# Kernel optimization log

Hardware: AMD Instinct MI355X
Metric: run time of the kernel (lower is better)

## Reference

```python
import jax, jax.numpy as jnp
import numpy as np

CUTOFF = 6.0
NWAVE = 12
NTYPE = 2
DIMS = [36, 256, 128, 64, 32, 1]  # norbit -> hidden -> output


def setup_inputs() -> dict:
    key = jax.random.key(0)
    N, K = 8192, 48
    M = N * K
    ks = jax.random.split(key, 16)
    cart = jax.random.uniform(ks[0], (N, 3), jnp.float32, 0.0, 40.0)
    species = jax.random.randint(ks[1], (N,), 0, NTYPE).astype(jnp.int32)
    center = jnp.repeat(jnp.arange(N, dtype=jnp.int32), K)          # row 0: center atom i
    off = jax.random.randint(ks[2], (M,), 1, N).astype(jnp.int32)
    neigh = jnp.mod(center + off, N)                                 # row 1: neighbor j != i
    neigh_list = jnp.stack([center, neigh], axis=0)
    shifts = jax.random.normal(ks[3], (M, 3), jnp.float32)           # PBC shift vectors
    rs = jnp.tile(jnp.linspace(0.0, CUTOFF, NWAVE, dtype=jnp.float32), (NTYPE, 1))
    inta = -0.5 * jnp.ones((NTYPE, NWAVE), jnp.float32)              # gaussian exponents (negative)
    cparams = jnp.ones((NTYPE, NWAVE), jnp.float32)                  # embedded-atom coefficients
    params = {}
    kidx = 4
    for i in range(4):  # 4 hidden layers, stacked over [3 nets, ntype]
        fi, fo = DIMS[i], DIMS[i + 1]
        params[f'w{i+1}'] = jax.random.normal(ks[kidx], (3, NTYPE, fi, fo), jnp.float32) / np.sqrt(fi)
        params[f'b{i+1}'] = jnp.zeros((3, NTYPE, fo), jnp.float32)
        params[f'a{i+1}'] = jnp.ones((3, NTYPE, fo), jnp.float32)    # Relu_like alpha
        params[f'g{i+1}'] = jnp.ones((3, NTYPE, fo), jnp.float32)    # Relu_like beta
        kidx += 1
    params['wout'] = jax.random.normal(ks[kidx], (3, NTYPE, DIMS[4], 1), jnp.float32) / np.sqrt(DIMS[4])
    params['bout'] = jnp.zeros((3, NTYPE, 1), jnp.float32)
    return dict(cart=cart, shifts=shifts, rs=rs, inta=inta, cparams=cparams,
                **params, species=species, neigh_list=neigh_list)


def density_fn(cart, shifts, rs, inta, cparams, species, neigh_list):
    # EANN GetDensity: radial gaussians * cosine cutoff * angular monomials, scattered to centers.
    N = cart.shape[0]
    i, j = neigh_list[0], neigh_list[1]
    dvec = cart[i] - cart[j] + shifts                                 # [M,3]
    dist = jnp.linalg.norm(dvec, axis=-1)                             # [M]
    fc = jnp.square(0.5 * jnp.cos(dist * (jnp.pi / CUTOFF)) + 0.5)    # cutoff_cosine
    # angular basis: L=0 (1), L=1 (3), L=2 (9) -> 13 components, each premultiplied by fc
    ang = jnp.concatenate([
        fc[:, None],
        fc[:, None] * dvec,
        fc[:, None] * (dvec[:, :, None] * dvec[:, None, :]).reshape(-1, 9),
    ], axis=1)                                                        # [M,13]
    sj = species[j]
    gauss = jnp.exp(inta[sj] * jnp.square(dist[:, None] - rs[sj])) * cparams[sj]  # [M,NWAVE]
    worb = ang[:, :, None] * gauss[:, None, :]                        # [M,13,NWAVE]
    B = jax.ops.segment_sum(worb, i, num_segments=N)                  # [N,13,NWAVE]
    d0 = jnp.square(B[:, 0])                                          # L=0
    d1 = jnp.sum(jnp.square(B[:, 1:4]), axis=1)                       # L=1
    d2 = jnp.sum(jnp.square(B[:, 4:13]), axis=1)                      # L=2
    return jnp.concatenate([d0, d1, d2], axis=1)                      # [N,36]


def net_energy(density, species, layers, wout, bout):
    # per-atom-type MLP with Relu_like activation a*silu(g*x); run all types, select by species
    T = wout.shape[0]
    h = jnp.broadcast_to(density, (T,) + density.shape)               # [T,N,36]
    for (w, b, a, g) in layers:
        h = jnp.einsum('tnf,tfo->tno', h, w) + b[:, None, :]
        h = a[:, None, :] * jax.nn.silu(g[:, None, :] * h)
    out = jnp.einsum('tnf,tfo->tno', h, wout) + bout[:, None, :]      # [T,N,1]
    per_atom = jnp.take_along_axis(out[..., 0].T, species[:, None].astype(jnp.int32), axis=1)[:, 0]
    return jnp.sum(per_atom)


def reference(cart, shifts, rs, inta, cparams,
              w1, b1, a1, g1, w2, b2, a2, g2, w3, b3, a3, g3, w4, b4, a4, g4,
              wout, bout, species, neigh_list):
    def energy(c, n):
        d = density_fn(c, shifts, rs, inta, cparams, species, neigh_list)
        layers = [(w1[n], b1[n], a1[n], g1[n]), (w2[n], b2[n], a2[n], g2[n]),
                  (w3[n], b3[n], a3[n], g3[n]), (w4[n], b4[n], a4[n], g4[n])]
        return net_energy(d, species, layers, wout[n], bout[n])

    jab1 = jax.grad(lambda c: energy(c, 0))(cart)                     # dE0/dcart (create_graph analogue)
    jab2 = jax.grad(lambda c: energy(c, 1))(cart)                     # dE1/dcart
    e2 = energy(cart, 2)
    polar = jnp.einsum('ij,ik->jk', cart, jab1)
    polar = polar + polar.T + jnp.einsum('ij,ik->jk', jab2, jab2)
    polar = polar + e2 * jnp.eye(3, dtype=polar.dtype)
    return polar
```

## Files before the change

### kernel.cpp

```cpp
#include <hip/hip_runtime.h>

#define NWAVE 12
#define NL 13
#define NBW (NL*NWAVE)
#define D0 36
#define D1 256
#define D2 128
#define D3 64
#define D4 32
#define AT 16
#define NMAX 8192
#define NBSC 128
#define PI6 0.52359877559829887307f

#define F4(p) (*(const float4*)(p))
#define F2(p) (*(const float2*)(p))

__device__ __forceinline__ float wave_reduce(float v){
  #pragma unroll
  for(int o=32;o>0;o>>=1) v += __shfl_down(v,o);
  return v;
}

__global__ void perm_kernel(const int* __restrict__ species, int* __restrict__ perm,
                            int* __restrict__ counts, int N){
  __shared__ int sc[256];
  int t = threadIdx.x;
  int per = N/256;
  int c0 = 0;
  for(int k=0;k<per;k++) c0 += (species[t*per+k]==0) ? 1 : 0;
  sc[t]=c0; __syncthreads();
  for(int off=1; off<256; off<<=1){
    int add = (t>=off)? sc[t-off] : 0;
    __syncthreads();
    sc[t] += add;
    __syncthreads();
  }
  int incl = sc[t];
  int excl = incl - c0;
  int total0 = sc[255];
  if(t==0){ counts[0]=total0; counts[1]=N-total0; }
  int base0 = excl;
  int base1 = N + (t*per - excl);
  for(int k=0;k<per;k++){
    int a = t*per+k;
    if(species[a]==0) perm[base0++]=a; else perm[base1++]=a;
  }
}

__global__ void transpose_kernel(const float* __restrict__ src, float* __restrict__ dst,
                                 int fi, int fo, int cpb){
  int slab = blockIdx.x / cpb;
  int chunk = blockIdx.x % cpb;
  int idx = chunk*256 + threadIdx.x;
  int E = fi*fo;
  if(idx < E){
    int f = idx / fo, o = idx % fo;
    dst[slab*E + o*fi + f] = src[slab*E + idx];
  }
}

__global__ void pairs_kernel(const float* __restrict__ cart, const float* __restrict__ shifts,
                             const int* __restrict__ species, const int* __restrict__ neighJ,
                             float4* __restrict__ pairbuf, int M, int N, int K){
  extern __shared__ float4 ca[];
  int t = threadIdx.x;
  for(int a=t; a<N; a+=blockDim.x)
    ca[a] = make_float4(cart[a*3+0], cart[a*3+1], cart[a*3+2], (float)species[a]);
  __syncthreads();
  int stride = gridDim.x*blockDim.x;
  for(int m = blockIdx.x*blockDim.x + t; m < M; m += stride){
    int i = m / K;
    int j = neighJ[m];
    float4 cj = ca[j];
    float4 ci = ca[i];
    float dx = ci.x - cj.x + shifts[m*3+0];
    float dy = ci.y - cj.y + shifts[m*3+1];
    float dz = ci.z - cj.z + shifts[m*3+2];
    float dist = sqrtf(dx*dx+dy*dy+dz*dz);
    float enc = (cj.w != 0.f) ? -dist : dist;
    pairbuf[m] = make_float4(dx, dy, dz, enc);
  }
}

__launch_bounds__(64)
__global__ void density_kernel(const float4* __restrict__ pairbuf,
                               const float* __restrict__ rs, const float* __restrict__ inta,
                               const float* __restrict__ cparams,
                               float* __restrict__ B, int K){
  int i = blockIdx.x;
  int t = threadIdx.x;
  __shared__ float sang[64][NL];
  __shared__ float sg[64][NWAVE];
  if(t < K){
    float4 pb = pairbuf[(size_t)i*K + t];
    float dx = pb.x, dy = pb.y, dz = pb.z;
    int sj = (pb.w < 0.f) ? 1 : 0;
    float dist = fabsf(pb.w);
    float base = 0.5f*cosf(dist*PI6)+0.5f;
    float fc = base*base;
    #pragma unroll
    for(int w=0;w<NWAVE;w++){
      float d = dist - rs[sj*NWAVE+w];
      sg[t][w] = __expf(inta[sj*NWAVE+w]*d*d)*cparams[sj*NWAVE+w];
    }
    sang[t][0]=fc;
    sang[t][1]=fc*dx;  sang[t][2]=fc*dy;  sang[t][3]=fc*dz;
    sang[t][4]=fc*dx*dx; sang[t][5]=fc*dx*dy; sang[t][6]=fc*dx*dz;
    sang[t][7]=fc*dy*dx; sang[t][8]=fc*dy*dy; sang[t][9]=fc*dy*dz;
    sang[t][10]=fc*dz*dx; sang[t][11]=fc*dz*dy; sang[t][12]=fc*dz*dz;
  }
  __syncthreads();
  for(int idx=t; idx<NBW; idx+=64){
    int l = idx/NWAVE, w = idx%NWAVE;
    float s = 0.f;
    for(int k=0;k<K;k++) s += sang[k][l]*sg[k][w];
    B[i*NBW+idx] = s;
  }
}

__launch_bounds__(256, 1)
__global__ void mlp_kernel(const float* __restrict__ B,
    const int* __restrict__ perm, const int* __restrict__ counts,
    const float* __restrict__ w1,const float* __restrict__ b1,const float* __restrict__ a1,const float* __restrict__ g1,
    const float* __restrict__ w2,const float* __restrict__ b2,const float* __restrict__ a2,const float* __restrict__ g2,
    const float* __restrict__ w3,const float* __restrict__ b3,const float* __restrict__ a3,const float* __restrict__ g3,
    const float* __restrict__ w4,const float* __restrict__ b4,const float* __restrict__ a4,const float* __restrict__ g4,
    const float* __restrict__ wout,const float* __restrict__ bout,
    const float* __restrict__ wt1,const float* __restrict__ wt2,const float* __restrict__ wt3,const float* __restrict__ wt4,
    float* __restrict__ G1, float* __restrict__ G2, float* __restrict__ e2acc, int N)
{
  const int bpt = N/AT;
  const int net = blockIdx.x / (2*bpt);
  const int rem = blockIdx.x % (2*bpt);
  const int typ = rem / bpt;
  const int sbase = (rem % bpt)*AT;
  const int cnt = counts[typ];
  if(sbase >= cnt) return;
  const int tid = threadIdx.x;
  const int slab = net*2 + typ;

  __shared__ __align__(16) float X[AT][D0];
  __shared__ __align__(16) float H1s[AT*D1];
  __shared__ __align__(16) float H2s[AT*D2];
  __shared__ __align__(16) float H3s[AT*D3];
  __shared__ __align__(16) float H4s[AT*D4];
  __shared__ int atomsS[AT];

  if(tid < AT){
    int slot = sbase + tid;
    atomsS[tid] = (slot < cnt) ? perm[typ*N + slot] : -1;
  }
  __syncthreads();

  for(int idx=tid; idx<AT*D0; idx+=256){
    int r = idx/D0, f = idx%D0;
    int a = atomsS[r];
    float v = 0.f;
    if(a >= 0){
      int w = f%NWAVE, grp = f/NWAVE;
      const float* Br = B + a*NBW;
      if(grp==0){ float b0=Br[w]; v=b0*b0; }
      else if(grp==1){
        #pragma unroll
        for(int l=1;l<4;l++){ float b0=Br[l*NWAVE+w]; v += b0*b0; }
      } else {
        #pragma unroll
        for(int l=4;l<13;l++){ float b0=Br[l*NWAVE+w]; v += b0*b0; }
      }
    }
    X[r][f] = v;
  }
  __syncthreads();

  const int l1c = (tid & 63)*4,  l1r = (tid >> 6)*4;
  const int l2c = (tid & 63)*2,  l2r = (tid >> 6)*4;
  const int l3c = (tid & 31)*2,  l3r = (tid >> 5)*2;
  const int l4c = (tid & 31),    l4r = (tid >> 5)*2;

  float A1r[4][4], A2r[4][2], A3r[2][2], A4r[2];

  {
    const float* W = w1 + slab*D0*D1;
    float acc[4][4];
    {
      float4 bv = F4(&b1[slab*D1+l1c]);
      #pragma unroll
      for(int rr=0;rr<4;rr++){ acc[rr][0]=bv.x; acc[rr][1]=bv.y; acc[rr][2]=bv.z; acc[rr][3]=bv.w; }
    }
    #pragma unroll
    for(int kk=0; kk<D0/4; kk++){
      float4 wa = F4(&W[(kk*4+0)*D1+l1c]);
      float4 wb = F4(&W[(kk*4+1)*D1+l1c]);
      float4 wc = F4(&W[(kk*4+2)*D1+l1c]);
      float4 wd = F4(&W[(kk*4+3)*D1+l1c]);
      #pragma unroll
      for(int rr=0;rr<4;rr++){
        float4 xv = F4(&X[l1r+rr][kk*4]);
        acc[rr][0] += xv.x*wa.x + xv.y*wb.x + xv.z*wc.x + xv.w*wd.x;
        acc[rr][1] += xv.x*wa.y + xv.y*wb.y + xv.z*wc.y + xv.w*wd.y;
        acc[rr][2] += xv.x*wa.z + xv.y*wb.z + xv.z*wc.z + xv.w*wd.z;
        acc[rr][3] += xv.x*wa.w + xv.y*wb.w + xv.z*wc.w + xv.w*wd.w;
      }
    }
    float4 av4 = F4(&a1[slab*D1+l1c]);
    float4 gv4 = F4(&g1[slab*D1+l1c]);
    float avv[4] = {av4.x, av4.y, av4.z, av4.w};
    float gvv[4] = {gv4.x, gv4.y, gv4.z, gv4.w};
    #pragma unroll
    for(int rr=0;rr<4;rr++){
      float4 h;
      float hp[4];
      #pragma unroll
      for(int cc=0;cc<4;cc++){
        float u = gvv[cc]*acc[rr][cc];
        float s = 1.f/(1.f+__expf(-u));
        hp[cc] = avv[cc]*u*s;
        A1r[rr][cc] = avv[cc]*gvv[cc]*s*(1.f + u*(1.f-s));
      }
      h.x=hp[0]; h.y=hp[1]; h.z=hp[2]; h.w=hp[3];
      *(float4*)&H1s[(l1r+rr)*D1 + l1c] = h;
    }
  }
  __syncthreads();
  {
    const float* W = w2 + slab*D1*D2;
    float acc[4][2];
    {
      float2 bv = F2(&b2[slab*D2+l2c]);
      #pragma unroll
      for(int rr=0;rr<4;rr++){ acc[rr][0]=bv.x; acc[rr][1]=bv.y; }
    }
    for(int kk=0; kk<D1/4; kk++){
      float2 wa = F2(&W[(kk*4+0)*D2+l2c]);
      float2 wb = F2(&W[(kk*4+1)*D2+l2c]);
      float2 wc = F2(&W[(kk*4+2)*D2+l2c]);
      float2 wd = F2(&W[(kk*4+3)*D2+l2c]);
      #pragma unroll
      for(int rr=0;rr<4;rr++){
        float4 hv = F4(&H1s[(l2r+rr)*D1 + kk*4]);
        acc[rr][0] += hv.x*wa.x + hv.y*wb.x + hv.z*wc.x + hv.w*wd.x;
        acc[rr][1] += hv.x*wa.y + hv.y*wb.y + hv.z*wc.y + hv.w*wd.y;
      }
    }
    float2 av2 = F2(&a2[slab*D2+l2c]);
    float2 gv2 = F2(&g2[slab*D2+l2c]);
    float avv[2] = {av2.x, av2.y};
    float gvv[2] = {gv2.x, gv2.y};
    #pragma unroll
    for(int rr=0;rr<4;rr++){
      float hp[2];
      #pragma unroll
      for(int cc=0;cc<2;cc++){
        float u = gvv[cc]*acc[rr][cc];
        float s = 1.f/(1.f+__expf(-u));
        hp[cc] = avv[cc]*u*s;
        A2r[rr][cc] = avv[cc]*gvv[cc]*s*(1.f + u*(1.f-s));
      }
      float2 h; h.x=hp[0]; h.y=hp[1];
      *(float2*)&H2s[(l2r+rr)*D2 + l2c] = h;
    }
  }
  __syncthreads();
  {
    const float* W = w3 + slab*D2*D3;
    float acc[2][2];
    {
      float2 bv = F2(&b3[slab*D3+l3c]);
      #pragma unroll
      for(int rr=0;rr<2;rr++){ acc[rr][0]=bv.x; acc[rr][1]=bv.y; }
    }
    for(int kk=0; kk<D2/4; kk++){
      float2 wa = F2(&W[(kk*4+0)*D3+l3c]);
      float2 wb = F2(&W[(kk*4+1)*D3+l3c]);
      float2 wc = F2(&W[(kk*4+2)*D3+l3c]);
      float2 wd = F2(&W[(kk*4+3)*D3+l3c]);
      #pragma unroll
      for(int rr=0;rr<2;rr++){
        float4 hv = F4(&H2s[(l3r+rr)*D2 + kk*4]);
        acc[rr][0] += hv.x*wa.x + hv.y*wb.x + hv.z*wc.x + hv.w*wd.x;
        acc[rr][1] += hv.x*wa.y + hv.y*wb.y + hv.z*wc.y + hv.w*wd.y;
      }
    }
    float2 av2 = F2(&a3[slab*D3+l3c]);
    float2 gv2 = F2(&g3[slab*D3+l3c]);
    float avv[2] = {av2.x, av2.y};
    float gvv[2] = {gv2.x, gv2.y};
    #pragma unroll
    for(int rr=0;rr<2;rr++){
      float hp[2];
      #pragma unroll
      for(int cc=0;cc<2;cc++){
        float u = gvv[cc]*acc[rr][cc];
        float s = 1.f/(1.f+__expf(-u));
        hp[cc] = avv[cc]*u*s;
        A3r[rr][cc] = avv[cc]*gvv[cc]*s*(1.f + u*(1.f-s));
      }
      float2 h; h.x=hp[0]; h.y=hp[1];
      *(float2*)&H3s[(l3r+rr)*D3 + l3c] = h;
    }
  }
  __syncthreads();
  {
    const float* W = w4 + slab*D3*D4;
    float bias = b4[slab*D4+l4c];
    float acc[2] = {bias, bias};
    for(int kk=0; kk<D3/4; kk++){
      float wa = W[(kk*4+0)*D4+l4c];
      float wb = W[(kk*4+1)*D4+l4c];
      float wc = W[(kk*4+2)*D4+l4c];
      float wd = W[(kk*4+3)*D4+l4c];
      #pragma unroll
      for(int rr=0;rr<2;rr++){
        float4 hv = F4(&H3s[(l4r+rr)*D3 + kk*4]);
        acc[rr] += hv.x*wa + hv.y*wb + hv.z*wc + hv.w*wd;
      }
    }
    float av = a4[slab*D4+l4c], gv = g4[slab*D4+l4c];
    #pragma unroll
    for(int rr=0;rr<2;rr++){
      float u = gv*acc[rr];
      float s = 1.f/(1.f+__expf(-u));
      H4s[(l4r+rr)*D4+l4c] = av*u*s;
      A4r[rr] = av*gv*s*(1.f + u*(1.f-s));
    }
  }
  __syncthreads();
  {
    const float* wo = wout + slab*D4;
    float val = 0.f;
    if(tid < AT){
      float s = bout[slab];
      const float* hr = &H4s[tid*D4];
      #pragma unroll
      for(int f=0;f<D4;f++) s += hr[f]*wo[f];
      if(net==2 && atomsS[tid]>=0) val = s;
    }
    if(net==2 && tid < 64){
      float v = wave_reduce(val);
      if(tid==0) atomicAdd(e2acc, v);
    }
  }
  if(net < 2){
    float* __restrict__ Gout = (net==0)? G1 : G2;
    const float* wo = wout + slab*D4;
    __syncthreads();
    {
      float wv = wo[l4c];
      H3s[(l4r+0)*D4+l4c] = wv * A4r[0];
      H3s[(l4r+1)*D4+l4c] = wv * A4r[1];
    }
    __syncthreads();
    {
      const float* WT = wt4 + slab*D4*D3;
      float acc[2][2] = {{0.f,0.f},{0.f,0.f}};
      #pragma unroll
      for(int kk=0; kk<D4/4; kk++){
        float2 wa = F2(&WT[(kk*4+0)*D3+l3c]);
        float2 wb = F2(&WT[(kk*4+1)*D3+l3c]);
        float2 wc = F2(&WT[(kk*4+2)*D3+l3c]);
        float2 wd = F2(&WT[(kk*4+3)*D3+l3c]);
        #pragma unroll
        for(int rr=0;rr<2;rr++){
          float4 dv = F4(&H3s[(l3r+rr)*D4 + kk*4]);
          acc[rr][0] += dv.x*wa.x + dv.y*wb.x + dv.z*wc.x + dv.w*wd.x;
          acc[rr][1] += dv.x*wa.y + dv.y*wb.y + dv.z*wc.y + dv.w*wd.y;
        }
      }
      #pragma unroll
      for(int rr=0;rr<2;rr++){
        float2 h;
        h.x = acc[rr][0]*A3r[rr][0];
        h.y = acc[rr][1]*A3r[rr][1];
        *(float2*)&H1s[(l3r+rr)*D3 + l3c] = h;
      }
    }
    __syncthreads();
    {
      const float* WT = wt3 + slab*D3*D2;
      float acc[4][2] = {{0.f,0.f},{0.f,0.f},{0.f,0.f},{0.f,0.f}};
      for(int kk=0; kk<D3/4; kk++){
        float2 wa = F2(&WT[(kk*4+0)*D2+l2c]);
        float2 wb = F2(&WT[(kk*4+1)*D2+l2c]);
        float2 wc = F2(&WT[(kk*4+2)*D2+l2c]);
        float2 wd = F2(&WT[(kk*4+3)*D2+l2c]);
        #pragma unroll
        for(int rr=0;rr<4;rr++){
          float4 dv = F4(&H1s[(l2r+rr)*D3 + kk*4]);
          acc[rr][0] += dv.x*wa.x + dv.y*wb.x + dv.z*wc.x + dv.w*wd.x;
          acc[rr][1] += dv.x*wa.y + dv.y*wb.y + dv.z*wc.y + dv.w*wd.y;
        }
      }
      #pragma unroll
      for(int rr=0;rr<4;rr++){
        float2 h;
        h.x = acc[rr][0]*A2r[rr][0];
        h.y = acc[rr][1]*A2r[rr][1];
        *(float2*)&H2s[(l2r+rr)*D2 + l2c] = h;
      }
    }
    __syncthreads();
    {
      const float* WT = wt2 + slab*D2*D1;
      float acc[4][4];
      #pragma unroll
      for(int rr=0;rr<4;rr++){ acc[rr][0]=0.f; acc[rr][1]=0.f; acc[rr][2]=0.f; acc[rr][3]=0.f; }
      for(int kk=0; kk<D2/4; kk++){
        float4 wa = F4(&WT[(kk*4+0)*D1+l1c]);
        float4 wb = F4(&WT[(kk*4+1)*D1+l1c]);
        float4 wc = F4(&WT[(kk*4+2)*D1+l1c]);
        float4 wd = F4(&WT[(kk*4+3)*D1+l1c]);
        #pragma unroll
        for(int rr=0;rr<4;rr++){
          float4 dv = F4(&H2s[(l1r+rr)*D2 + kk*4]);
          acc[rr][0] += dv.x*wa.x + dv.y*wb.x + dv.z*wc.x + dv.w*wd.x;
          acc[rr][1] += dv.x*wa.y + dv.y*wb.y + dv.z*wc.y + dv.w*wd.y;
          acc[rr][2] += dv.x*wa.z + dv.y*wb.z + dv.z*wc.z + dv.w*wd.z;
          acc[rr][3] += dv.x*wa.w + dv.y*wb.w + dv.z*wc.w + dv.w*wd.w;
        }
      }
      #pragma unroll
      for(int rr=0;rr<4;rr++){
        float4 h;
        h.x = acc[rr][0]*A1r[rr][0];
        h.y = acc[rr][1]*A1r[rr][1];
        h.z = acc[rr][2]*A1r[rr][2];
        h.w = acc[rr][3]*A1r[rr][3];
        *(float4*)&H1s[(l1r+rr)*D1 + l1c] = h;
      }
    }
    __syncthreads();
    {
      const float* WT = wt1 + slab*D1*D0;
      for(int idx=tid; idx<AT*D0; idx+=256){
        int r = idx/D0, f = idx%D0;
        const float* dr = &H1s[r*D1];
        float acc = 0.f;
        for(int oo=0; oo<D1; oo+=4){
          const float4 dv = F4(&dr[oo]);
          acc += dv.x*WT[(oo+0)*D0+f] + dv.y*WT[(oo+1)*D0+f]
               + dv.z*WT[(oo+2)*D0+f] + dv.w*WT[(oo+3)*D0+f];
        }
        int a = atomsS[r];
        if(a >= 0) Gout[a*D0+f] = acc;
      }
    }
  }
}

__launch_bounds__(64)
__global__ void pair_back_kernel(const float4* __restrict__ pairbuf,
                                 const float* __restrict__ shifts,
                                 const float* __restrict__ rs, const float* __restrict__ inta,
                                 const float* __restrict__ cparams,
                                 const float* __restrict__ B,
                                 const float* __restrict__ G1, const float* __restrict__ G2,
                                 float* __restrict__ Ppart, float* __restrict__ jab2c,
                                 float* __restrict__ f2buf, int K){
  int i = blockIdx.x;
  int t = threadIdx.x;
  __shared__ float E1[NBW], E2[NBW];
  for(int idx=t; idx<NBW; idx+=64){
    int l = idx/NWAVE, w = idx%NWAVE;
    int grp = (l==0) ? 0 : ((l<4) ? 1 : 2);
    float b = B[i*NBW+idx];
    E1[idx] = 2.f*b*G1[i*D0 + grp*NWAVE + w];
    E2[idx] = 2.f*b*G2[i*D0 + grp*NWAVE + w];
  }
  __syncthreads();
  float p[9] = {0.f,0.f,0.f,0.f,0.f,0.f,0.f,0.f,0.f};
  float fi2[3] = {0.f,0.f,0.f};
  if(t < K){
    int m = i*K + t;
    float4 pb = pairbuf[(size_t)m];
    float dx = pb.x, dy = pb.y, dz = pb.z;
    int sj = (pb.w < 0.f) ? 1 : 0;
    float dist = fabsf(pb.w);
    float shx = shifts[m*3+0], shy = shifts[m*3+1], shz = shifts[m*3+2];
    float invd = 1.f/dist;
    float u = dist*PI6;
    float base = 0.5f*cosf(u)+0.5f;
    float fc = base*base;
    float fcp = -PI6*sinf(u)*base;
    float gs[NWAVE], tw[NWAVE];
    #pragma unroll
    for(int w=0;w<NWAVE;w++){
      float d = dist - rs[sj*NWAVE+w];
      float ia = inta[sj*NWAVE+w];
      float g = __expf(ia*d*d)*cparams[sj*NWAVE+w];
      gs[w] = g;
      tw[w] = fcp*g + fc*(2.f*ia*d*g);
    }
    float mono[NL] = {1.f, dx,dy,dz, dx*dx,dx*dy,dx*dz, dy*dx,dy*dy,dy*dz, dz*dx,dz*dy,dz*dz};
    float f1[3], f2[3];
    for(int net=0; net<2; net++){
      const float* E = net ? E2 : E1;
      float sl[NL];
      float radial = 0.f;
      #pragma unroll
      for(int l=0;l<NL;l++){
        float s = 0.f, q = 0.f;
        #pragma unroll
        for(int w=0;w<NWAVE;w++){
          float e = E[l*NWAVE+w];
          s += e*gs[w];
          q += e*tw[w];
        }
        sl[l] = s;
        radial += mono[l]*q;
      }
      float Ax = sl[1] + 2.f*sl[4]*dx + (sl[5]+sl[7])*dy + (sl[6]+sl[10])*dz;
      float Ay = sl[2] + (sl[5]+sl[7])*dx + 2.f*sl[8]*dy + (sl[9]+sl[11])*dz;
      float Az = sl[3] + (sl[6]+sl[10])*dx + (sl[9]+sl[11])*dy + 2.f*sl[12]*dz;
      float rr = radial*invd;
      float fx = dx*rr + fc*Ax;
      float fy = dy*rr + fc*Ay;
      float fz = dz*rr + fc*Az;
      if(net==0){ f1[0]=fx; f1[1]=fy; f1[2]=fz; }
      else      { f2[0]=fx; f2[1]=fy; f2[2]=fz; }
    }
    float cx = dx-shx, cy = dy-shy, cz = dz-shz;
    p[0]=cx*f1[0]; p[1]=cx*f1[1]; p[2]=cx*f1[2];
    p[3]=cy*f1[0]; p[4]=cy*f1[1]; p[5]=cy*f1[2];
    p[6]=cz*f1[0]; p[7]=cz*f1[1]; p[8]=cz*f1[2];
    float* fb = f2buf + (size_t)m*3;
    fb[0]=f2[0]; fb[1]=f2[1]; fb[2]=f2[2];
    fi2[0]=f2[0]; fi2[1]=f2[1]; fi2[2]=f2[2];
  }
  #pragma unroll
  for(int k=0;k<9;k++){
    float v = wave_reduce(p[k]);
    if(t==0) Ppart[(size_t)i*9+k] = v;
  }
  #pragma unroll
  for(int c=0;c<3;c++){
    float v = wave_reduce(fi2[c]);
    if(t==0) jab2c[(size_t)i*3+c] = v;
  }
}

__global__ void scatter_kernel(const int* __restrict__ neighJ, const float* __restrict__ f2buf,
                               float* __restrict__ jpart, int M, int N){
  __shared__ float lds[NMAX];
  int b = blockIdx.x, t = threadIdx.x;
  int chunk = (M + gridDim.x - 1) / gridDim.x;
  int m0 = b*chunk;
  int m1 = m0 + chunk; if(m1 > M) m1 = M;
  for(int c=0;c<3;c++){
    for(int n=t; n<N; n+=256) lds[n] = 0.f;
    __syncthreads();
    for(int m=m0+t; m<m1; m+=256)
      atomicAdd(&lds[neighJ[m]], -f2buf[(size_t)m*3+c]);
    __syncthreads();
    float* dst = jpart + ((size_t)b*3 + c)*N;
    for(int n=t; n<N; n+=256) dst[n] = lds[n];
    __syncthreads();
  }
}

__global__ void reduce_kernel(const float* __restrict__ Ppart, const float* __restrict__ jab2c,
                              const float* __restrict__ jpart,
                              float* __restrict__ Pacc, float* __restrict__ S2, int N){
  __shared__ float red[256];
  int tid = threadIdx.x;
  float s2[9] = {0.f,0.f,0.f,0.f,0.f,0.f,0.f,0.f,0.f};
  float pp[9] = {0.f,0.f,0.f,0.f,0.f,0.f,0.f,0.f,0.f};
  for(int n = blockIdx.x*256 + tid; n < N; n += gridDim.x*256){
    float x = jab2c[n*3+0], y = jab2c[n*3+1], z = jab2c[n*3+2];
    for(int b=0;b<NBSC;b++){
      const float* jp = jpart + (size_t)b*3*N;
      x += jp[0*(size_t)N + n];
      y += jp[1*(size_t)N + n];
      z += jp[2*(size_t)N + n];
    }
    s2[0]+=x*x; s2[1]+=x*y; s2[2]+=x*z;
    s2[3]+=y*x; s2[4]+=y*y; s2[5]+=y*z;
    s2[6]+=z*x; s2[7]+=z*y; s2[8]+=z*z;
    const float* pr = Ppart + (size_t)n*9;
    #pragma unroll
    for(int k=0;k<9;k++) pp[k] += pr[k];
  }
  #pragma unroll
  for(int k=0;k<9;k++){
    red[tid]=s2[k]; __syncthreads();
    for(int off=128; off>0; off>>=1){
      if(tid<off) red[tid]+=red[tid+off];
      __syncthreads();
    }
    if(tid==0) atomicAdd(&S2[k], red[0]);
    __syncthreads();
    red[tid]=pp[k]; __syncthreads();
    for(int off=128; off>0; off>>=1){
      if(tid<off) red[tid]+=red[tid+off];
      __syncthreads();
    }
    if(tid==0) atomicAdd(&Pacc[k], red[0]);
    __syncthreads();
  }
}

__global__ void final_kernel(const float* __restrict__ Pacc, const float* __restrict__ S2,
                             const float* __restrict__ e2acc, float* __restrict__ out){
  int tid = threadIdx.x;
  if(tid < 9){
    int a = tid/3, b = tid%3;
    float v = Pacc[a*3+b] + Pacc[b*3+a] + S2[tid];
    if(a==b) v += e2acc[0];
    out[tid] = v;
  }
}

extern "C" void kernel_launch(void* const* d_in, const int* in_sizes, int n_in,
                              void* d_out, int out_size, void* d_ws, size_t ws_size,
                              hipStream_t stream){
  const float* cart    = (const float*)d_in[0];
  const float* shifts  = (const float*)d_in[1];
  const float* rs      = (const float*)d_in[2];
  const float* inta    = (const float*)d_in[3];
  const float* cparams = (const float*)d_in[4];
  const float* w1 = (const float*)d_in[5];
  const float* b1 = (const float*)d_in[6];
  const float* a1 = (const float*)d_in[7];
  const float* g1 = (const float*)d_in[8];
  const float* w2 = (const float*)d_in[9];
  const float* b2 = (const float*)d_in[10];
  const float* a2 = (const float*)d_in[11];
  const float* g2 = (const float*)d_in[12];
  const float* w3 = (const float*)d_in[13];
  const float* b3 = (const float*)d_in[14];
  const float* a3 = (const float*)d_in[15];
  const float* g3 = (const float*)d_in[16];
  const float* w4 = (const float*)d_in[17];
  const float* b4 = (const float*)d_in[18];
  const float* a4 = (const float*)d_in[19];
  const float* g4 = (const float*)d_in[20];
  const float* wout = (const float*)d_in[21];
  const float* bout = (const float*)d_in[22];
  const int* species = (const int*)d_in[23];
  const int* neigh   = (const int*)d_in[24];
  float* out = (float*)d_out;

  const int N = in_sizes[0]/3;
  const int M = in_sizes[24]/2;
  const int K = M/N;
  const int* neighJ = neigh + M;

  char* base = (char*)d_ws;
  size_t off = 0;
  auto alloc = [&](size_t bytes)->void*{
    void* p = base + off;
    off = (off + bytes + 255) & ~(size_t)255;
    return p;
  };
  float*  Bws    = (float*)alloc((size_t)N*NBW*4);
  float*  G1ws   = (float*)alloc((size_t)N*D0*4);
  float*  G2ws   = (float*)alloc((size_t)N*D0*4);
  float*  Ppart  = (float*)alloc((size_t)N*9*4);
  float*  jab2c  = (float*)alloc((size_t)N*3*4);
  float*  f2buf  = (float*)alloc((size_t)M*3*4);
  float4* pairbuf= (float4*)alloc((size_t)M*16);
  float*  jpart  = (float*)alloc((size_t)NBSC*3*N*4);
  float*  acc    = (float*)alloc(32*4);
  int*    counts = (int*)alloc(2*4);
  int*    perm   = (int*)alloc((size_t)2*N*4);
  float*  WT1    = (float*)alloc((size_t)6*D0*D1*4);
  float*  WT2    = (float*)alloc((size_t)6*D1*D2*4);
  float*  WT3    = (float*)alloc((size_t)6*D2*D3*4);
  float*  WT4    = (float*)alloc((size_t)6*D3*D4*4);

  hipMemsetAsync(acc, 0, 32*4, stream);

  size_t ldsBytes = (size_t)N*16;
  hipFuncSetAttribute((const void*)pairs_kernel,
                      hipFuncAttributeMaxDynamicSharedMemorySize, (int)ldsBytes);

  perm_kernel<<<1,256,0,stream>>>(species, perm, counts, N);
  transpose_kernel<<<6*((D0*D1+255)/256),256,0,stream>>>(w1, WT1, D0, D1, (D0*D1+255)/256);
  transpose_kernel<<<6*((D1*D2+255)/256),256,0,stream>>>(w2, WT2, D1, D2, (D1*D2+255)/256);
  transpose_kernel<<<6*((D2*D3+255)/256),256,0,stream>>>(w3, WT3, D2, D3, (D2*D3+255)/256);
  transpose_kernel<<<6*((D3*D4+255)/256),256,0,stream>>>(w4, WT4, D3, D4, (D3*D4+255)/256);
  pairs_kernel<<<256,1024,ldsBytes,stream>>>(cart, shifts, species, neighJ, pairbuf, M, N, K);
  density_kernel<<<N,64,0,stream>>>(pairbuf, rs, inta, cparams, Bws, K);
  mlp_kernel<<<3*2*(N/AT),256,0,stream>>>(Bws, perm, counts,
      w1,b1,a1,g1, w2,b2,a2,g2, w3,b3,a3,g3, w4,b4,a4,g4, wout,bout,
      WT1,WT2,WT3,WT4, G1ws,G2ws, acc+18, N);
  pair_back_kernel<<<N,64,0,stream>>>(pairbuf, shifts, rs, inta, cparams,
                                      Bws, G1ws, G2ws, Ppart, jab2c, f2buf, K);
  scatter_kernel<<<NBSC,256,0,stream>>>(neighJ, f2buf, jpart, M, N);
  reduce_kernel<<<64,256,0,stream>>>(Ppart, jab2c, jpart, acc, acc+9, N);
  final_kernel<<<1,64,0,stream>>>(acc, acc+9, acc+18, out);
}
```

Measured before the change: 324.2 us.

## Double MLP block threads to 512 and merge weight transposes into one launch

The MLP kernel now runs 512 threads per block instead of 256. Each thread handles half as many atom rows in every forward and backward layer, which raises parallelism and cuts per-thread register use; the launch bounds change to (512,4) so more blocks can share a compute unit. The four weight-transpose launches are merged into one kernel that picks its layer by global index, removing three launch overheads. The cost is less register-level reuse of each weight load across rows, so more weight traffic goes to global memory or cache.

```diff
diff --git a/kernel.cpp b/kernel.cpp
--- a/kernel.cpp
+++ b/kernel.cpp
@@ -48,15 +48,28 @@
   }
 }
 
-__global__ void transpose_kernel(const float* __restrict__ src, float* __restrict__ dst,
-                                 int fi, int fo, int cpb){
-  int slab = blockIdx.x / cpb;
-  int chunk = blockIdx.x % cpb;
-  int idx = chunk*256 + threadIdx.x;
-  int E = fi*fo;
-  if(idx < E){
-    int f = idx / fo, o = idx % fo;
-    dst[slab*E + o*fi + f] = src[slab*E + idx];
+__global__ void transpose_all_kernel(const float* __restrict__ w1, const float* __restrict__ w2,
+                                     const float* __restrict__ w3, const float* __restrict__ w4,
+                                     float* __restrict__ t1, float* __restrict__ t2,
+                                     float* __restrict__ t3, float* __restrict__ t4){
+  const int E1 = 6*D0*D1, E2 = 6*D1*D2, E3 = 6*D2*D3, E4 = 6*D3*D4;
+  int idx = blockIdx.x*256 + threadIdx.x;
+  if(idx < E1){
+    int slab = idx/(D0*D1), r = idx%(D0*D1);
+    int f = r/D1, o = r%D1;
+    t1[slab*D0*D1 + o*D0 + f] = w1[idx];
+  } else if(idx < E1+E2){
+    int k = idx-E1; int slab = k/(D1*D2), r = k%(D1*D2);
+    int f = r/D2, o = r%D2;
+    t2[slab*D1*D2 + o*D1 + f] = w2[k];
+  } else if(idx < E1+E2+E3){
+    int k = idx-E1-E2; int slab = k/(D2*D3), r = k%(D2*D3);
+    int f = r/D3, o = r%D3;
+    t3[slab*D2*D3 + o*D2 + f] = w3[k];
+  } else if(idx < E1+E2+E3+E4){
+    int k = idx-E1-E2-E3; int slab = k/(D3*D4), r = k%(D3*D4);
+    int f = r/D4, o = r%D4;
+    t4[slab*D3*D4 + o*D3 + f] = w4[k];
   }
 }
 
@@ -119,7 +132,7 @@
   }
 }
 
-__launch_bounds__(256, 1)
+__launch_bounds__(512, 4)
 __global__ void mlp_kernel(const float* __restrict__ B,
     const int* __restrict__ perm, const int* __restrict__ counts,
     const float* __restrict__ w1,const float* __restrict__ b1,const float* __restrict__ a1,const float* __restrict__ g1,
@@ -153,7 +166,7 @@
   }
   __syncthreads();
 
-  for(int idx=tid; idx<AT*D0; idx+=256){
+  for(int idx=tid; idx<AT*D0; idx+=512){
     int r = idx/D0, f = idx%D0;
     int a = atomsS[r];
     float v = 0.f;
@@ -173,20 +186,20 @@
   }
   __syncthreads();
 
-  const int l1c = (tid & 63)*4,  l1r = (tid >> 6)*4;
-  const int l2c = (tid & 63)*2,  l2r = (tid >> 6)*4;
-  const int l3c = (tid & 31)*2,  l3r = (tid >> 5)*2;
-  const int l4c = (tid & 31),    l4r = (tid >> 5)*2;
-
-  float A1r[4][4], A2r[4][2], A3r[2][2], A4r[2];
+  const int l1c = (tid & 63)*4,  l1r = (tid >> 6)*2;
+  const int l2c = (tid & 63)*2,  l2r = (tid >> 6)*2;
+  const int l3c = (tid & 31)*2,  l3r = (tid >> 5);
+  const int l4c = (tid & 31),    l4r = (tid >> 5);
+
+  float A1r[2][4], A2r[2][2], A3r[2], A4r;
 
   {
     const float* W = w1 + slab*D0*D1;
-    float acc[4][4];
+    float acc[2][4];
     {
       float4 bv = F4(&b1[slab*D1+l1c]);
       #pragma unroll
-      for(int rr=0;rr<4;rr++){ acc[rr][0]=bv.x; acc[rr][1]=bv.y; acc[rr][2]=bv.z; acc[rr][3]=bv.w; }
+      for(int rr=0;rr<2;rr++){ acc[rr][0]=bv.x; acc[rr][1]=bv.y; acc[rr][2]=bv.z; acc[rr][3]=bv.w; }
     }
     #pragma unroll
     for(int kk=0; kk<D0/4; kk++){
@@ -195,7 +208,7 @@
       float4 wc = F4(&W[(kk*4+2)*D1+l1c]);
       float4 wd = F4(&W[(kk*4+3)*D1+l1c]);
       #pragma unroll
-      for(int rr=0;rr<4;rr++){
+      for(int rr=0;rr<2;rr++){
         float4 xv = F4(&X[l1r+rr][kk*4]);
         acc[rr][0] += xv.x*wa.x + xv.y*wb.x + xv.z*wc.x + xv.w*wd.x;
         acc[rr][1] += xv.x*wa.y + xv.y*wb.y + xv.z*wc.y + xv.w*wd.y;
@@ -208,8 +221,7 @@
     float avv[4] = {av4.x, av4.y, av4.z, av4.w};
     float gvv[4] = {gv4.x, gv4.y, gv4.z, gv4.w};
     #pragma unroll
-    for(int rr=0;rr<4;rr++){
-      float4 h;
+    for(int rr=0;rr<2;rr++){
       float hp[4];
       #pragma unroll
       for(int cc=0;cc<4;cc++){
@@ -218,18 +230,18 @@
         hp[cc] = avv[cc]*u*s;
         A1r[rr][cc] = avv[cc]*gvv[cc]*s*(1.f + u*(1.f-s));
       }
-      h.x=hp[0]; h.y=hp[1]; h.z=hp[2]; h.w=hp[3];
+      float4 h; h.x=hp[0]; h.y=hp[1]; h.z=hp[2]; h.w=hp[3];
       *(float4*)&H1s[(l1r+rr)*D1 + l1c] = h;
     }
   }
   __syncthreads();
   {
     const float* W = w2 + slab*D1*D2;
-    float acc[4][2];
+    float acc[2][2];
     {
       float2 bv = F2(&b2[slab*D2+l2c]);
       #pragma unroll
-      for(int rr=0;rr<4;rr++){ acc[rr][0]=bv.x; acc[rr][1]=bv.y; }
+      for(int rr=0;rr<2;rr++){ acc[rr][0]=bv.x; acc[rr][1]=bv.y; }
     }
     for(int kk=0; kk<D1/4; kk++){
       float2 wa = F2(&W[(kk*4+0)*D2+l2c]);
@@ -237,7 +249,7 @@
       float2 wc = F2(&W[(kk*4+2)*D2+l2c]);
       float2 wd = F2(&W[(kk*4+3)*D2+l2c]);
       #pragma unroll
-      for(int rr=0;rr<4;rr++){
+      for(int rr=0;rr<2;rr++){
         float4 hv = F4(&H1s[(l2r+rr)*D1 + kk*4]);
         acc[rr][0] += hv.x*wa.x + hv.y*wb.x + hv.z*wc.x + hv.w*wd.x;
         acc[rr][1] += hv.x*wa.y + hv.y*wb.y + hv.z*wc.y + hv.w*wd.y;
@@ -248,7 +260,7 @@
     float avv[2] = {av2.x, av2.y};
     float gvv[2] = {gv2.x, gv2.y};
     #pragma unroll
-    for(int rr=0;rr<4;rr++){
+    for(int rr=0;rr<2;rr++){
       float hp[2];
       #pragma unroll
       for(int cc=0;cc<2;cc++){
@@ -264,66 +276,52 @@
   __syncthreads();
   {
     const float* W = w3 + slab*D2*D3;
-    float acc[2][2];
+    float acc[2];
     {
       float2 bv = F2(&b3[slab*D3+l3c]);
-      #pragma unroll
-      for(int rr=0;rr<2;rr++){ acc[rr][0]=bv.x; acc[rr][1]=bv.y; }
+      acc[0]=bv.x; acc[1]=bv.y;
     }
     for(int kk=0; kk<D2/4; kk++){
       float2 wa = F2(&W[(kk*4+0)*D3+l3c]);
       float2 wb = F2(&W[(kk*4+1)*D3+l3c]);
       float2 wc = F2(&W[(kk*4+2)*D3+l3c]);
       float2 wd = F2(&W[(kk*4+3)*D3+l3c]);
-      #pragma unroll
-      for(int rr=0;rr<2;rr++){
-        float4 hv = F4(&H2s[(l3r+rr)*D2 + kk*4]);
-        acc[rr][0] += hv.x*wa.x + hv.y*wb.x + hv.z*wc.x + hv.w*wd.x;
-        acc[rr][1] += hv.x*wa.y + hv.y*wb.y + hv.z*wc.y + hv.w*wd.y;
-      }
+      float4 hv = F4(&H2s[l3r*D2 + kk*4]);
+      acc[0] += hv.x*wa.x + hv.y*wb.x + hv.z*wc.x + hv.w*wd.x;
+      acc[1] += hv.x*wa.y + hv.y*wb.y + hv.z*wc.y + hv.w*wd.y;
     }
     float2 av2 = F2(&a3[slab*D3+l3c]);
     float2 gv2 = F2(&g3[slab*D3+l3c]);
     float avv[2] = {av2.x, av2.y};
     float gvv[2] = {gv2.x, gv2.y};
+    float hp[2];
     #pragma unroll
-    for(int rr=0;rr<2;rr++){
-      float hp[2];
-      #pragma unroll
-      for(int cc=0;cc<2;cc++){
-        float u = gvv[cc]*acc[rr][cc];
-        float s = 1.f/(1.f+__expf(-u));
-        hp[cc] = avv[cc]*u*s;
-        A3r[rr][cc] = avv[cc]*gvv[cc]*s*(1.f + u*(1.f-s));
-      }
-      float2 h; h.x=hp[0]; h.y=hp[1];
-      *(float2*)&H3s[(l3r+rr)*D3 + l3c] = h;
-    }
+    for(int cc=0;cc<2;cc++){
+      float u = gvv[cc]*acc[cc];
+      float s = 1.f/(1.f+__expf(-u));
+      hp[cc] = avv[cc]*u*s;
+      A3r[cc] = avv[cc]*gvv[cc]*s*(1.f + u*(1.f-s));
+    }
+    float2 h; h.x=hp[0]; h.y=hp[1];
+    *(float2*)&H3s[l3r*D3 + l3c] = h;
   }
   __syncthreads();
   {
     const float* W = w4 + slab*D3*D4;
-    float bias = b4[slab*D4+l4c];
-    float acc[2] = {bias, bias};
+    float acc = b4[slab*D4+l4c];
     for(int kk=0; kk<D3/4; kk++){
       float wa = W[(kk*4+0)*D4+l4c];
       float wb = W[(kk*4+1)*D4+l4c];
       float wc = W[(kk*4+2)*D4+l4c];
       float wd = W[(kk*4+3)*D4+l4c];
-      #pragma unroll
-      for(int rr=0;rr<2;rr++){
-        float4 hv = F4(&H3s[(l4r+rr)*D3 + kk*4]);
-        acc[rr] += hv.x*wa + hv.y*wb + hv.z*wc + hv.w*wd;
-      }
+      float4 hv = F4(&H3s[l4r*D3 + kk*4]);
+      acc += hv.x*wa + hv.y*wb + hv.z*wc + hv.w*wd;
     }
     float av = a4[slab*D4+l4c], gv = g4[slab*D4+l4c];
-    #pragma unroll
-    for(int rr=0;rr<2;rr++){
-      float u = gv*acc[rr];
-      float s = 1.f/(1.f+__expf(-u));
-      H4s[(l4r+rr)*D4+l4c] = av*u*s;
-      A4r[rr] = av*gv*s*(1.f + u*(1.f-s));
-    }
+    float u = gv*acc;
+    float s = 1.f/(1.f+__expf(-u));
+    H4s[l4r*D4+l4c] = av*u*s;
+    A4r = av*gv*s*(1.f + u*(1.f-s));
   }
   __syncthreads();
   {
@@ -345,54 +343,44 @@
     float* __restrict__ Gout = (net==0)? G1 : G2;
     const float* wo = wout + slab*D4;
     __syncthreads();
-    {
-      float wv = wo[l4c];
-      H3s[(l4r+0)*D4+l4c] = wv * A4r[0];
-      H3s[(l4r+1)*D4+l4c] = wv * A4r[1];
-    }
+    H3s[l4r*D4+l4c] = wo[l4c] * A4r;
     __syncthreads();
     {
       const float* WT = wt4 + slab*D4*D3;
-      float acc[2][2] = {{0.f,0.f},{0.f,0.f}};
+      float acc[2] = {0.f,0.f};
       #pragma unroll
       for(int kk=0; kk<D4/4; kk++){
         float2 wa = F2(&WT[(kk*4+0)*D3+l3c]);
         float2 wb = F2(&WT[(kk*4+1)*D3+l3c]);
         float2 wc = F2(&WT[(kk*4+2)*D3+l3c]);
         float2 wd = F2(&WT[(kk*4+3)*D3+l3c]);
-        #pragma unroll
-        for(int rr=0;rr<2;rr++){
-          float4 dv = F4(&H3s[(l3r+rr)*D4 + kk*4]);
-          acc[rr][0] += dv.x*wa.x + dv.y*wb.x + dv.z*wc.x + dv.w*wd.x;
-          acc[rr][1] += dv.x*wa.y + dv.y*wb.y + dv.z*wc.y + dv.w*wd.y;
-        }
-      }
-      #pragma unroll
-      for(int rr=0;rr<2;rr++){
-        float2 h;
-        h.x = acc[rr][0]*A3r[rr][0];
-        h.y = acc[rr][1]*A3r[rr][1];
-        *(float2*)&H1s[(l3r+rr)*D3 + l3c] = h;
-      }
+        float4 dv = F4(&H3s[l3r*D4 + kk*4]);
+        acc[0] += dv.x*wa.x + dv.y*wb.x + dv.z*wc.x + dv.w*wd.x;
+        acc[1] += dv.x*wa.y + dv.y*wb.y + dv.z*wc.y + dv.w*wd.y;
+      }
+      float2 h;
+      h.x = acc[0]*A3r[0];
+      h.y = acc[1]*A3r[1];
+      *(float2*)&H1s[l3r*D3 + l3c] = h;
     }
     __syncthreads();
     {
       const float* WT = wt3 + slab*D3*D2;
-      float acc[4][2] = {{0.f,0.f},{0.f,0.f},{0.f,0.f},{0.f,0.f}};
+      float acc[2][2] = {{0.f,0.f},{0.f,0.f}};
       for(int kk=0; kk<D3/4; kk++){
         float2 wa = F2(&WT[(kk*4+0)*D2+l2c]);
         float2 wb = F2(&WT[(kk*4+1)*D2+l2c]);
         float2 wc = F2(&WT[(kk*4+2)*D2+l2c]);
         float2 wd = F2(&WT[(kk*4+3)*D2+l2c]);
         #pragma unroll
-        for(int rr=0;rr<4;rr++){
+        for(int rr=0;rr<2;rr++){
           float4 dv = F4(&H1s[(l2r+rr)*D3 + kk*4]);
           acc[rr][0] += dv.x*wa.x + dv.y*wb.x + dv.z*wc.x + dv.w*wd.x;
           acc[rr][1] += dv.x*wa.y + dv.y*wb.y + dv.z*wc.y + dv.w*wd.y;
         }
       }
       #pragma unroll
-      for(int rr=0;rr<4;rr++){
+      for(int rr=0;rr<2;rr++){
         float2 h;
         h.x = acc[rr][0]*A2r[rr][0];
         h.y = acc[rr][1]*A2r[rr][1];
@@ -402,16 +390,16 @@
     __syncthreads();
     {
       const float* WT = wt2 + slab*D2*D1;
-      float acc[4][4];
-      #pragma unroll
-      for(int rr=0;rr<4;rr++){ acc[rr][0]=0.f; acc[rr][1]=0.f; acc[rr][2]=0.f; acc[rr][3]=0.f; }
+      float acc[2][4];
+      #pragma unroll
+      for(int rr=0;rr<2;rr++){ acc[rr][0]=0.f; acc[rr][1]=0.f; acc[rr][2]=0.f; acc[rr][3]=0.f; }
       for(int kk=0; kk<D2/4; kk++){
         float4 wa = F4(&WT[(kk*4+0)*D1+l1c]);
         float4 wb = F4(&WT[(kk*4+1)*D1+l1c]);
         float4 wc = F4(&WT[(kk*4+2)*D1+l1c]);
         float4 wd = F4(&WT[(kk*4+3)*D1+l1c]);
         #pragma unroll
-        for(int rr=0;rr<4;rr++){
+        for(int rr=0;rr<2;rr++){
           float4 dv = F4(&H2s[(l1r+rr)*D2 + kk*4]);
           acc[rr][0] += dv.x*wa.x + dv.y*wb.x + dv.z*wc.x + dv.w*wd.x;
           acc[rr][1] += dv.x*wa.y + dv.y*wb.y + dv.z*wc.y + dv.w*wd.y;
@@ -420,7 +408,7 @@
         }
       }
       #pragma unroll
-      for(int rr=0;rr<4;rr++){
+      for(int rr=0;rr<2;rr++){
         float4 h;
         h.x = acc[rr][0]*A1r[rr][0];
         h.y = acc[rr][1]*A1r[rr][1];
@@ -432,7 +420,7 @@
     __syncthreads();
     {
       const float* WT = wt1 + slab*D1*D0;
-      for(int idx=tid; idx<AT*D0; idx+=256){
+      for(int idx=tid; idx<AT*D0; idx+=512){
         int r = idx/D0, f = idx%D0;
         const float* dr = &H1s[r*D1];
         float acc = 0.f;
@@ -674,14 +662,12 @@
   hipFuncSetAttribute((const void*)pairs_kernel,
                       hipFuncAttributeMaxDynamicSharedMemorySize, (int)ldsBytes);
 
+  const int ETOT = 6*(D0*D1 + D1*D2 + D2*D3 + D3*D4);
   perm_kernel<<<1,256,0,stream>>>(species, perm, counts, N);
-  transpose_kernel<<<6*((D0*D1+255)/256),256,0,stream>>>(w1, WT1, D0, D1, (D0*D1+255)/256);
-  transpose_kernel<<<6*((D1*D2+255)/256),256,0,stream>>>(w2, WT2, D1, D2, (D1*D2+255)/256);
-  transpose_kernel<<<6*((D2*D3+255)/256),256,0,stream>>>(w3, WT3, D2, D3, (D2*D3+255)/256);
-  transpose_kernel<<<6*((D3*D4+255)/256),256,0,stream>>>(w4, WT4, D3, D4, (D3*D4+255)/256);
+  transpose_all_kernel<<<(ETOT+255)/256,256,0,stream>>>(w1,w2,w3,w4, WT1,WT2,WT3,WT4);
   pairs_kernel<<<256,1024,ldsBytes,stream>>>(cart, shifts, species, neighJ, pairbuf, M, N, K);
   density_kernel<<<N,64,0,stream>>>(pairbuf, rs, inta, cparams, Bws, K);
-  mlp_kernel<<<3*2*(N/AT),256,0,stream>>>(Bws, perm, counts,
+  mlp_kernel<<<3*2*(N/AT),512,0,stream>>>(Bws, perm, counts,
       w1,b1,a1,g1, w2,b2,a2,g2, w3,b3,a3,g3, w4,b4,a4,g4, wout,bout,
       WT1,WT2,WT3,WT4, G1ws,G2ws, acc+18, N);
   pair_back_kernel<<<N,64,0,stream>>>(pairbuf, shifts, rs, inta, cparams,
```

After: 422.4 us. +30.3%, slower.
